# Performance work log

Hardware: AMD Instinct MI355X
Metric: run time of the kernel (lower is better)

Reference implementation:

```python
import jax, jax.numpy as jnp
import numpy as np

N = 100000
E = 1600000
IN_C = 128
OUT_C = 128


def setup_inputs() -> dict:
    key = jax.random.key(0)
    k1, k2, k3, k4, k5, k6 = jax.random.split(key, 6)
    x = jax.random.normal(k1, (N, IN_C), dtype=jnp.float32)
    edge_row = jax.random.randint(k2, (E,), 0, N, dtype=jnp.int32)  # dst nodes
    edge_col = jax.random.randint(k3, (E,), 0, N, dtype=jnp.int32)  # src nodes
    scale = 1.0 / np.sqrt(IN_C)
    W_l = jax.random.normal(k4, (IN_C, OUT_C), dtype=jnp.float32) * scale
    b_l = jax.random.normal(k5, (OUT_C,), dtype=jnp.float32) * 0.01
    W_r = jax.random.normal(k6, (IN_C, OUT_C), dtype=jnp.float32) * scale
    return {"x": x, "edge_row": edge_row, "edge_col": edge_col,
            "W_l": W_l, "b_l": b_l, "W_r": W_r}


def reference(x, edge_row, edge_col, W_l, b_l, W_r):
    # SAGEConv with mean aggregation over adj_t (edge_row=dst, edge_col=src)
    msgs = x[edge_col]                                   # [E, IN_C] gather
    summed = jax.ops.segment_sum(msgs, edge_row, num_segments=N)  # [N, IN_C]
    deg = jax.ops.segment_sum(jnp.ones((E,), dtype=x.dtype), edge_row,
                              num_segments=N)            # [N]
    agg = summed / jnp.maximum(deg, 1.0)[:, None]        # mean aggregation
    out = agg @ W_l + b_l + x @ W_r                      # lin_l(agg) + lin_r(x_dst)
    return jax.nn.relu(out)
```

## Files before the change

kernel.cpp:

```cpp
#include <hip/hip_runtime.h>

#define N_NODES 100000
#define E_EDGES 1600000
#define C 128
#define BSHIFT 9
#define BMASK 511
#define BNODES 512
#define NBKT 196
#define CAP 9728

#define PA_BLOCKS 782
#define PACK_BLOCKS 8
#define CVT_BLOCKS 3125

typedef __attribute__((ext_vector_type(8))) short short8;
typedef __attribute__((ext_vector_type(4))) float f32x4;

__device__ __forceinline__ unsigned short f2bf(float f) {
  unsigned int b = __float_as_uint(f);
  return (unsigned short)((b + 0x7fffu + ((b >> 16) & 1u)) >> 16);
}
__device__ __forceinline__ float bflo(unsigned int v) {
  return __uint_as_float(v << 16);
}
__device__ __forceinline__ float bfhi(unsigned int v) {
  return __uint_as_float(v & 0xffff0000u);
}

__global__ __launch_bounds__(512) void mega_kernel(
    const float* __restrict__ x, const int* __restrict__ erow,
    const int* __restrict__ ecol, const float* __restrict__ W_l,
    const float* __restrict__ W_r, ushort* __restrict__ xh,
    ushort* __restrict__ Bp, int* __restrict__ bcnt, int* __restrict__ pairs) {
  __shared__ int cnt[NBKT], pos[NBKT], loff[NBKT], total;
  __shared__ int lbuf[2048];
  __shared__ int gaddr[2048];
  int bid = blockIdx.x;
  int tid = threadIdx.x;

  if (bid < PA_BLOCKS) {
    for (int b = tid; b < NBKT; b += 512) cnt[b] = 0;
    __syncthreads();

    int idx = bid * 512 + tid;
    bool ok = (idx < E_EDGES / 4);
    int4 r, c;
    int bk[4], rk[4];
    if (ok) {
      r = ((const int4*)erow)[idx];
      c = ((const int4*)ecol)[idx];
      bk[0] = r.x >> BSHIFT; rk[0] = atomicAdd(&cnt[bk[0]], 1);
      bk[1] = r.y >> BSHIFT; rk[1] = atomicAdd(&cnt[bk[1]], 1);
      bk[2] = r.z >> BSHIFT; rk[2] = atomicAdd(&cnt[bk[2]], 1);
      bk[3] = r.w >> BSHIFT; rk[3] = atomicAdd(&cnt[bk[3]], 1);
    }
    __syncthreads();

    if (tid < NBKT) pos[tid] = atomicAdd(&bcnt[tid], cnt[tid]);
    if (tid == 0) {
      int run = 0;
      for (int b = 0; b < NBKT; ++b) { loff[b] = run; run += cnt[b]; }
      total = run;
    }
    __syncthreads();

    if (ok) {
      int src[4] = {c.x, c.y, c.z, c.w};
      int dst[4] = {r.x, r.y, r.z, r.w};
#pragma unroll
      for (int i = 0; i < 4; ++i) {
        int s = loff[bk[i]] + rk[i];
        lbuf[s] = (src[i] << BSHIFT) | (dst[i] & BMASK);
        int g = pos[bk[i]] + rk[i];
        gaddr[s] = (g < CAP) ? bk[i] * CAP + g : -1;
      }
    }
    __syncthreads();

    int tot = total;
    for (int i = tid; i < tot; i += 512) {
      int g = gaddr[i];
      if (g >= 0) pairs[g] = lbuf[i];
    }
  } else if (bid < PA_BLOCKS + PACK_BLOCKS) {
    int t = (bid - PA_BLOCKS) * 512 + tid;
    int Cb = t >> 9, kb = (t >> 6) & 7, lane = t & 63;
    int n = Cb * 16 + (lane & 15);
    int k0 = kb * 32 + (lane >> 4) * 8;
    ushort u[8];
#pragma unroll
    for (int j = 0; j < 8; ++j) {
      int k = k0 + j;
      float w = (k < C) ? W_l[k * C + n] : W_r[(k - C) * C + n];
      u[j] = f2bf(w);
    }
    ((uint4*)Bp)[t] = *(const uint4*)u;
  } else {
    int t = (bid - PA_BLOCKS - PACK_BLOCKS) * 512 + tid;
    float4 a = ((const float4*)x)[2 * t];
    float4 b = ((const float4*)x)[2 * t + 1];
    ushort u[8] = {f2bf(a.x), f2bf(a.y), f2bf(a.z), f2bf(a.w),
                   f2bf(b.x), f2bf(b.y), f2bf(b.z), f2bf(b.w)};
    ((uint4*)xh)[t] = *(const uint4*)u;
  }
}

__global__ __launch_bounds__(512) void passB_kernel(
    const int* __restrict__ pairs, const int* __restrict__ bcnt,
    int* __restrict__ off, int* __restrict__ ssrc) {
  __shared__ int l[512];
  __shared__ int cur[512];
  __shared__ int s_gbase;
  int b = blockIdx.x, t = threadIdx.x;

  int v = 0;
  if (t < 256) {
    v = (t < NBKT) ? min(bcnt[t], CAP) : 0;
    l[t] = v;
  }
  __syncthreads();
  for (int d = 1; d < 256; d <<= 1) {
    int u = (t >= d && t < 256) ? l[t - d] : 0;
    __syncthreads();
    if (t < 256) l[t] += u;
    __syncthreads();
  }
  if (t == b) s_gbase = l[t] - v;
  __syncthreads();

  int nbase = b << BSHIFT;
  int nn = min(BNODES, N_NODES - nbase);
  int cntb = min(bcnt[b], CAP);
  int gbase = s_gbase;
  const int* bp = pairs + b * CAP;

  l[t] = 0;
  __syncthreads();
  for (int e = t; e < cntb; e += 512) atomicAdd(&l[bp[e] & BMASK], 1);
  __syncthreads();
  int own = l[t];
  for (int d = 1; d < 512; d <<= 1) {
    int u = (t >= d) ? l[t - d] : 0;
    __syncthreads();
    l[t] += u;
    __syncthreads();
  }
  int excl = l[t] - own;
  if (t < nn) { off[nbase + t] = gbase + excl; cur[t] = excl; }
  if (b == NBKT - 1 && t == 511) off[N_NODES] = gbase + l[511];
  __syncthreads();
  for (int e = t; e < cntb; e += 512) {
    int p = bp[e];
    int posn = atomicAdd(&cur[p & BMASK], 1);
    ssrc[gbase + posn] = p >> BSHIFT;
  }
}

__global__ __launch_bounds__(256) void fused_kernel(
    const ushort* __restrict__ xh, const int* __restrict__ off,
    const int* __restrict__ ssrc, const ushort* __restrict__ Bp,
    const float* __restrict__ b_l, float* __restrict__ out) {
  __shared__ ushort lA[32][264];
  int tid = threadIdx.x;
  int lane = tid & 63;
  int wave = tid >> 6;
  long base = (long)blockIdx.x * 32;

  for (int i = tid; i < 32 * 16; i += 256) {
    int r = i >> 4, q = i & 15;
    uint4 v = ((const uint4*)(xh + (base + r) * C))[q];
    *(uint4*)&lA[r][128 + q * 8] = v;
  }

  int l4 = lane & 15;
  int q = lane >> 4;

  for (int j = 0; j < 8; ++j) {
    int n = wave * 8 + j;
    long row = base + n;
    int e0 = off[row];
    int e1 = off[row + 1];
    float s[8];
#pragma unroll
    for (int i = 0; i < 8; ++i) s[i] = 0.0f;

    int e = e0 + q;
    for (; e + 4 < e1; e += 8) {
      int sa = ssrc[e];
      int sb = ssrc[e + 4];
      uint4 va = ((const uint4*)(xh + (long)sa * C))[l4];
      uint4 vb = ((const uint4*)(xh + (long)sb * C))[l4];
      s[0] += bflo(va.x) + bflo(vb.x); s[1] += bfhi(va.x) + bfhi(vb.x);
      s[2] += bflo(va.y) + bflo(vb.y); s[3] += bfhi(va.y) + bfhi(vb.y);
      s[4] += bflo(va.z) + bflo(vb.z); s[5] += bfhi(va.z) + bfhi(vb.z);
      s[6] += bflo(va.w) + bflo(vb.w); s[7] += bfhi(va.w) + bfhi(vb.w);
    }
    if (e < e1) {
      int sa = ssrc[e];
      uint4 va = ((const uint4*)(xh + (long)sa * C))[l4];
      s[0] += bflo(va.x); s[1] += bfhi(va.x);
      s[2] += bflo(va.y); s[3] += bfhi(va.y);
      s[4] += bflo(va.z); s[5] += bfhi(va.z);
      s[6] += bflo(va.w); s[7] += bfhi(va.w);
    }
#pragma unroll
    for (int i = 0; i < 8; ++i) {
      s[i] += __shfl_xor(s[i], 16);
      s[i] += __shfl_xor(s[i], 32);
    }
    float inv = 1.0f / fmaxf((float)(e1 - e0), 1.0f);
    if (q == 0) {
      ushort u[8];
#pragma unroll
      for (int i = 0; i < 8; ++i) u[i] = f2bf(s[i] * inv);
      *(uint4*)&lA[n][l4 * 8] = *(const uint4*)u;
    }
  }
  __syncthreads();

  f32x4 acc0 = {0, 0, 0, 0}, acc1 = {0, 0, 0, 0};
  f32x4 acc2 = {0, 0, 0, 0}, acc3 = {0, 0, 0, 0};
  int m = lane & 15, quad = lane >> 4;
  const ushort* bp0 = Bp + (((2 * wave + 0) * 8) * 64 + lane) * 8;
  const ushort* bp1 = Bp + (((2 * wave + 1) * 8) * 64 + lane) * 8;
#pragma unroll
  for (int kb = 0; kb < 8; ++kb) {
    short8 a0 = *(const short8*)&lA[m][kb * 32 + quad * 8];
    short8 a1 = *(const short8*)&lA[16 + m][kb * 32 + quad * 8];
    short8 b0 = *(const short8*)(bp0 + kb * 64 * 8);
    short8 b1 = *(const short8*)(bp1 + kb * 64 * 8);
    acc0 = __builtin_amdgcn_mfma_f32_16x16x32_bf16(a0, b0, acc0, 0, 0, 0);
    acc1 = __builtin_amdgcn_mfma_f32_16x16x32_bf16(a0, b1, acc1, 0, 0, 0);
    acc2 = __builtin_amdgcn_mfma_f32_16x16x32_bf16(a1, b0, acc2, 0, 0, 0);
    acc3 = __builtin_amdgcn_mfma_f32_16x16x32_bf16(a1, b1, acc3, 0, 0, 0);
  }

  int col0 = (2 * wave + 0) * 16 + m;
  int col1 = col0 + 16;
  float bl0 = b_l[col0], bl1 = b_l[col1];
#pragma unroll
  for (int r = 0; r < 4; ++r) {
    long row0 = base + quad * 4 + r;
    long row1 = row0 + 16;
    out[row0 * C + col0] = fmaxf(acc0[r] + bl0, 0.0f);
    out[row0 * C + col1] = fmaxf(acc1[r] + bl1, 0.0f);
    out[row1 * C + col0] = fmaxf(acc2[r] + bl0, 0.0f);
    out[row1 * C + col1] = fmaxf(acc3[r] + bl1, 0.0f);
  }
}

extern "C" void kernel_launch(void* const* d_in, const int* in_sizes, int n_in,
                              void* d_out, int out_size, void* d_ws, size_t ws_size,
                              hipStream_t stream) {
  const float* x   = (const float*)d_in[0];
  const int* erow  = (const int*)d_in[1];
  const int* ecol  = (const int*)d_in[2];
  const float* W_l = (const float*)d_in[3];
  const float* b_l = (const float*)d_in[4];
  const float* W_r = (const float*)d_in[5];
  float* out = (float*)d_out;

  char* p = (char*)d_ws;
  ushort* xh  = (ushort*)p;  p += (size_t)N_NODES * C * 2;
  ushort* Bp  = (ushort*)p;  p += 2 * C * C * 2;
  int* off    = (int*)p;     p += (size_t)(N_NODES + 4) * 4;
  int* pairs  = (int*)p;     p += (size_t)NBKT * CAP * 4;
  int* ssrc   = (int*)p;     p += (size_t)E_EDGES * 4;
  int* bcnt   = (int*)p;

  hipMemsetAsync(bcnt, 0, NBKT * sizeof(int), stream);
  mega_kernel<<<PA_BLOCKS + PACK_BLOCKS + CVT_BLOCKS, 512, 0, stream>>>(
      x, erow, ecol, W_l, W_r, xh, Bp, bcnt, pairs);
  passB_kernel<<<NBKT, 512, 0, stream>>>(pairs, bcnt, off, ssrc);
  fused_kernel<<<N_NODES / 32, 256, 0, stream>>>(xh, off, ssrc, Bp, b_l, out);
}
```

Baseline: 222.3 us.

## Batch more edges per bucketing block and cache bucket pairs in LDS

Each pass-A block of the bucketing kernel now handles 8 edges per thread instead of 4, which halves the block count and the number of global atomics on the bucket counters. The serial per-block bucket offset loop becomes a parallel shared-memory scan. passB now runs 1024 threads per block and stages each bucket's pairs in LDS, so the second scatter pass reads shared memory instead of global memory. The cost is more shared memory per block and more barriers in the scans, which may lower occupancy.

```diff
diff --git a/kernel.cpp b/kernel.cpp
--- a/kernel.cpp
+++ b/kernel.cpp
@@ -9,7 +9,7 @@
 #define NBKT 196
 #define CAP 9728
 
-#define PA_BLOCKS 782
+#define PA_BLOCKS 391
 #define PACK_BLOCKS 8
 #define CVT_BLOCKS 3125
 
@@ -32,9 +32,9 @@
     const int* __restrict__ ecol, const float* __restrict__ W_l,
     const float* __restrict__ W_r, ushort* __restrict__ xh,
     ushort* __restrict__ Bp, int* __restrict__ bcnt, int* __restrict__ pairs) {
-  __shared__ int cnt[NBKT], pos[NBKT], loff[NBKT], total;
-  __shared__ int lbuf[2048];
-  __shared__ int gaddr[2048];
+  __shared__ int cnt[NBKT], pos[NBKT], loff[256], total;
+  __shared__ int lbuf[4096];
+  __shared__ int gaddr[4096];
   int bid = blockIdx.x;
   int tid = threadIdx.x;
 
@@ -42,37 +42,66 @@
     for (int b = tid; b < NBKT; b += 512) cnt[b] = 0;
     __syncthreads();
 
-    int idx = bid * 512 + tid;
-    bool ok = (idx < E_EDGES / 4);
-    int4 r, c;
-    int bk[4], rk[4];
-    if (ok) {
-      r = ((const int4*)erow)[idx];
-      c = ((const int4*)ecol)[idx];
-      bk[0] = r.x >> BSHIFT; rk[0] = atomicAdd(&cnt[bk[0]], 1);
-      bk[1] = r.y >> BSHIFT; rk[1] = atomicAdd(&cnt[bk[1]], 1);
-      bk[2] = r.z >> BSHIFT; rk[2] = atomicAdd(&cnt[bk[2]], 1);
-      bk[3] = r.w >> BSHIFT; rk[3] = atomicAdd(&cnt[bk[3]], 1);
-    }
-    __syncthreads();
-
-    if (tid < NBKT) pos[tid] = atomicAdd(&bcnt[tid], cnt[tid]);
-    if (tid == 0) {
-      int run = 0;
-      for (int b = 0; b < NBKT; ++b) { loff[b] = run; run += cnt[b]; }
-      total = run;
-    }
-    __syncthreads();
-
-    if (ok) {
-      int src[4] = {c.x, c.y, c.z, c.w};
-      int dst[4] = {r.x, r.y, r.z, r.w};
+    int i0 = bid * 1024 + tid;
+    int i1 = i0 + 512;
+    bool ok0 = (i0 < E_EDGES / 4), ok1 = (i1 < E_EDGES / 4);
+    int4 r0, c0, r1, c1;
+    int bk[8], rk[8];
+    if (ok0) {
+      r0 = ((const int4*)erow)[i0];
+      c0 = ((const int4*)ecol)[i0];
+      bk[0] = r0.x >> BSHIFT; rk[0] = atomicAdd(&cnt[bk[0]], 1);
+      bk[1] = r0.y >> BSHIFT; rk[1] = atomicAdd(&cnt[bk[1]], 1);
+      bk[2] = r0.z >> BSHIFT; rk[2] = atomicAdd(&cnt[bk[2]], 1);
+      bk[3] = r0.w >> BSHIFT; rk[3] = atomicAdd(&cnt[bk[3]], 1);
+    }
+    if (ok1) {
+      r1 = ((const int4*)erow)[i1];
+      c1 = ((const int4*)ecol)[i1];
+      bk[4] = r1.x >> BSHIFT; rk[4] = atomicAdd(&cnt[bk[4]], 1);
+      bk[5] = r1.y >> BSHIFT; rk[5] = atomicAdd(&cnt[bk[5]], 1);
+      bk[6] = r1.z >> BSHIFT; rk[6] = atomicAdd(&cnt[bk[6]], 1);
+      bk[7] = r1.w >> BSHIFT; rk[7] = atomicAdd(&cnt[bk[7]], 1);
+    }
+    __syncthreads();
+
+    int v = 0;
+    if (tid < 256) {
+      v = (tid < NBKT) ? cnt[tid] : 0;
+      loff[tid] = v;
+      if (tid < NBKT) pos[tid] = atomicAdd(&bcnt[tid], v);
+    }
+    __syncthreads();
+    for (int d = 1; d < 256; d <<= 1) {
+      int u = (tid < 256 && tid >= d) ? loff[tid - d] : 0;
+      __syncthreads();
+      if (tid < 256) loff[tid] += u;
+      __syncthreads();
+    }
+    if (tid < 256) loff[tid] -= v;
+    if (tid == NBKT - 1) total = loff[tid] + v;
+    __syncthreads();
+
+    if (ok0) {
+      int src[4] = {c0.x, c0.y, c0.z, c0.w};
+      int dst[4] = {r0.x, r0.y, r0.z, r0.w};
 #pragma unroll
       for (int i = 0; i < 4; ++i) {
         int s = loff[bk[i]] + rk[i];
         lbuf[s] = (src[i] << BSHIFT) | (dst[i] & BMASK);
         int g = pos[bk[i]] + rk[i];
         gaddr[s] = (g < CAP) ? bk[i] * CAP + g : -1;
+      }
+    }
+    if (ok1) {
+      int src[4] = {c1.x, c1.y, c1.z, c1.w};
+      int dst[4] = {r1.x, r1.y, r1.z, r1.w};
+#pragma unroll
+      for (int i = 0; i < 4; ++i) {
+        int s = loff[bk[4 + i]] + rk[4 + i];
+        lbuf[s] = (src[i] << BSHIFT) | (dst[i] & BMASK);
+        int g = pos[bk[4 + i]] + rk[4 + i];
+        gaddr[s] = (g < CAP) ? bk[4 + i] * CAP + g : -1;
       }
     }
     __syncthreads();
@@ -105,9 +134,10 @@
   }
 }
 
-__global__ __launch_bounds__(512) void passB_kernel(
+__global__ __launch_bounds__(1024) void passB_kernel(
     const int* __restrict__ pairs, const int* __restrict__ bcnt,
     int* __restrict__ off, int* __restrict__ ssrc) {
+  __shared__ int lds_pairs[CAP];
   __shared__ int l[512];
   __shared__ int cur[512];
   __shared__ int s_gbase;
@@ -116,16 +146,19 @@
   int v = 0;
   if (t < 256) {
     v = (t < NBKT) ? min(bcnt[t], CAP) : 0;
-    l[t] = v;
-  }
+    l[t < 512 ? t : 0] = 0;
+  }
+  __shared__ int bs[256];
+  if (t < 256) bs[t] = v;
   __syncthreads();
   for (int d = 1; d < 256; d <<= 1) {
-    int u = (t >= d && t < 256) ? l[t - d] : 0;
-    __syncthreads();
-    if (t < 256) l[t] += u;
-    __syncthreads();
-  }
-  if (t == b) s_gbase = l[t] - v;
+    int u = (t < 256 && t >= d) ? bs[t - d] : 0;
+    __syncthreads();
+    if (t < 256) bs[t] += u;
+    __syncthreads();
+  }
+  if (t == b) s_gbase = bs[t] - v;
+  if (t < 512) l[t] = 0;
   __syncthreads();
 
   int nbase = b << BSHIFT;
@@ -134,23 +167,30 @@
   int gbase = s_gbase;
   const int* bp = pairs + b * CAP;
 
-  l[t] = 0;
-  __syncthreads();
-  for (int e = t; e < cntb; e += 512) atomicAdd(&l[bp[e] & BMASK], 1);
-  __syncthreads();
-  int own = l[t];
+  for (int e = t; e < cntb; e += 1024) {
+    int p = bp[e];
+    lds_pairs[e] = p;
+    atomicAdd(&l[p & BMASK], 1);
+  }
+  __syncthreads();
+
+  int own = (t < 512) ? l[t] : 0;
   for (int d = 1; d < 512; d <<= 1) {
-    int u = (t >= d) ? l[t - d] : 0;
-    __syncthreads();
-    l[t] += u;
-    __syncthreads();
-  }
-  int excl = l[t] - own;
-  if (t < nn) { off[nbase + t] = gbase + excl; cur[t] = excl; }
-  if (b == NBKT - 1 && t == 511) off[N_NODES] = gbase + l[511];
-  __syncthreads();
-  for (int e = t; e < cntb; e += 512) {
-    int p = bp[e];
+    int u = (t < 512 && t >= d) ? l[t - d] : 0;
+    __syncthreads();
+    if (t < 512) l[t] += u;
+    __syncthreads();
+  }
+  if (t < 512) {
+    int excl = l[t] - own;
+    if (t < nn) off[nbase + t] = gbase + excl;
+    cur[t] = excl;
+  }
+  if (b == NBKT - 1 && t == 1023) off[N_NODES] = gbase + l[511];
+  __syncthreads();
+
+  for (int e = t; e < cntb; e += 1024) {
+    int p = lds_pairs[e];
     int posn = atomicAdd(&cur[p & BMASK], 1);
     ssrc[gbase + posn] = p >> BSHIFT;
   }
@@ -271,6 +311,6 @@
   hipMemsetAsync(bcnt, 0, NBKT * sizeof(int), stream);
   mega_kernel<<<PA_BLOCKS + PACK_BLOCKS + CVT_BLOCKS, 512, 0, stream>>>(
       x, erow, ecol, W_l, W_r, xh, Bp, bcnt, pairs);
-  passB_kernel<<<NBKT, 512, 0, stream>>>(pairs, bcnt, off, ssrc);
+  passB_kernel<<<NBKT, 1024, 0, stream>>>(pairs, bcnt, off, ssrc);
   fused_kernel<<<N_NODES / 32, 256, 0, stream>>>(xh, off, ssrc, Bp, b_l, out);
 }
```

Result: faster. 208.9 us (-6.0%).
